# Kernel optimization log

Measured on AMD Instinct MI355X. Metric: run time of the kernel, lower is better.

The kernel has to match this reference:

```python
import jax, jax.numpy as jnp
import numpy as np

H = 32          # num_heads
D = 64          # kv_channels (head dim)
HID = 2048      # hidden_size
MAXPOS = 2048   # max_seq_length


def _rotary_table(num_pos, dim):
    # [num_pos, dim]: sin for first dim/2 cols, cos for last dim/2 cols
    inv_freq = 1.0 / (10000.0 ** (jnp.arange(0, dim, 2, dtype=jnp.float32) / dim))
    t = jnp.arange(num_pos, dtype=jnp.float32)[:, None] * inv_freq[None, :]
    return jnp.concatenate([jnp.sin(t), jnp.cos(t)], axis=1)


def _apply_rope(x, sin, cos):
    # x: [B,S,H,D]; sin,cos: [B,S,D/2]
    sin = jnp.concatenate([sin, sin], axis=-1)[:, :, None, :]  # [B,S,1,D]
    cos = jnp.concatenate([cos, cos], axis=-1)[:, :, None, :]
    half = x.shape[-1] // 2
    x1, x2 = x[..., :half], x[..., half:]
    rot = jnp.concatenate([-x2, x1], axis=-1)
    return x * cos + rot * sin


def setup_inputs() -> dict:
    key = jax.random.key(0)
    k1, k2, k3, k4 = jax.random.split(key, 4)
    B, S = 2, 2048
    hidden_states = jax.random.normal(k1, (B, S, HID), jnp.float32)
    attention_mask = jax.random.randint(k2, (B, 1, S, S), 0, 2).astype(bool)
    position_ids = jnp.broadcast_to(jnp.arange(S, dtype=jnp.int32)[None, :], (B, S))
    W_qkv = jax.random.normal(k3, (3 * H * D, HID), jnp.float32) * 0.02
    W_o = jax.random.normal(k4, (HID, H * D), jnp.float32) * 0.02
    return {"hidden_states": hidden_states, "attention_mask": attention_mask,
            "position_ids": position_ids, "W_qkv": W_qkv, "W_o": W_o}


def reference(hidden_states, attention_mask, position_ids, W_qkv, W_o):
    B, S, _ = hidden_states.shape
    # fused QKV projection (nn.Linear: x @ W.T, no bias)
    qkv = hidden_states @ W_qkv.T                       # [B,S,3*H*D]
    qkv = qkv.reshape(B, S, H, 3 * D)
    q, k, v = jnp.split(qkv, 3, axis=-1)                # each [B,S,H,D]
    sincos = _rotary_table(MAXPOS, D)[position_ids]     # [B,S,D]
    sin, cos = jnp.split(sincos, 2, axis=-1)            # [B,S,D/2] each
    q = _apply_rope(q, sin, cos)
    k = _apply_rope(k, sin, cos)
    scale = jnp.sqrt(jnp.float32(D))
    scores = jnp.einsum('bqhd,bkhd->bhqk', q, k) / scale   # [B,H,S,S]
    scores = jnp.where(attention_mask, jnp.float32(-10000.0), scores)
    weights = jax.nn.softmax(scores, axis=-1)
    attn = jnp.einsum('bhqk,bkhd->bqhd', weights, v)       # [B,S,H,D]
    attn = attn.reshape(B, S, H * D)
    return attn @ W_o.T                                    # [B,S,HID]
```

## Files before the change

kernel.cpp:

```cpp
#include <hip/hip_runtime.h>

#define B_   2
#define S_   2048
#define H_   32
#define D_   64
#define HID_ 2048

typedef unsigned short ushort_t;
typedef __attribute__((ext_vector_type(8))) short short8;
typedef __attribute__((ext_vector_type(4))) float floatx4;

typedef const __attribute__((address_space(1))) char* gas_ptr;
typedef __attribute__((address_space(3))) char* las_ptr;

__device__ __forceinline__ float bf2f(ushort_t u) {
    union { unsigned int i; float f; } v; v.i = ((unsigned int)u) << 16; return v.f;
}
__device__ __forceinline__ ushort_t f2bf(float f) {
    union { float f; unsigned int i; } v; v.f = f;
    unsigned int x = v.i;
    unsigned int r = x + 0x7fffu + ((x >> 16) & 1u);
    return (ushort_t)(r >> 16);
}

__device__ __forceinline__ float fexp2(float x) {
#if __has_builtin(__builtin_amdgcn_exp2f)
    return __builtin_amdgcn_exp2f(x);
#else
    float r; asm("v_exp_f32 %0, %1" : "=v"(r) : "v"(x)); return r;
#endif
}

__device__ __forceinline__ unsigned cvt_pk_bf16(float a, float b) {
    unsigned r;
    asm("v_cvt_pk_bf16_f32 %0, %1, %2" : "=v"(r) : "v"(a), "v"(b));
    return r;
}

__global__ __launch_bounds__(256) void cast3_f32_bf16(const float* __restrict__ in0, ushort_t* __restrict__ out0, int n0,
                                                      const float* __restrict__ in1, ushort_t* __restrict__ out1, int n1,
                                                      const float* __restrict__ in2, ushort_t* __restrict__ out2, int n2) {
    int i = blockIdx.x * 256 + threadIdx.x;
    const float* in; ushort_t* out;
    if (i < n0)            { in = in0; out = out0; }
    else if (i < n0 + n1)  { in = in1; out = out1; i -= n0; }
    else if (i < n0 + n1 + n2) { in = in2; out = out2; i -= n0 + n1; }
    else return;
    const float4* p = (const float4*)(in + (size_t)i * 8);
    float4 a = p[0], b = p[1];
    uint4 o;
    o.x = cvt_pk_bf16(a.x, a.y);
    o.y = cvt_pk_bf16(a.z, a.w);
    o.z = cvt_pk_bf16(b.x, b.y);
    o.w = cvt_pk_bf16(b.z, b.w);
    *(uint4*)(out + (size_t)i * 8) = o;
}

__global__ __launch_bounds__(256) void mask_pack(const int* __restrict__ m,
                                                 unsigned long long* __restrict__ bits) {
    int idx = blockIdx.x * 256 + threadIdx.x;
    unsigned long long bal = __ballot(m[idx] != 0);
    if ((threadIdx.x & 63) == 0) bits[idx >> 6] = bal;
}

__global__ __launch_bounds__(512, 2) void gemm256_bt(const ushort_t* __restrict__ A,
                                                     const ushort_t* __restrict__ Bm,
                                                     ushort_t* __restrict__ C,
                                                     int M, int N, int K) {
    __shared__ ushort_t lA[2][256][64];
    __shared__ ushort_t lB[2][256][64];
    const int tid  = threadIdx.x;
    const int w    = tid >> 6, lane = tid & 63;
    const int quad = lane >> 4, l16 = lane & 15;
    const int wm = w >> 2, wn = w & 3;
    const int sr = lane >> 3, ss = lane & 7;
    const int gseg = (ss ^ sr) * 8;

    const int nbx = N >> 8;
    int id  = blockIdx.x;
    int cpx = gridDim.x >> 3;
    int swz = (id & 7) * cpx + (id >> 3);
    int by = swz / nbx, bx = swz - by * nbx;
    const int m0 = by * 256, n0 = bx * 256;

    int arow[2], brow[2];
    arow[0] = w * 8;                       arow[1] = 128 + w * 8;
    brow[0] = (w >> 2) * 64 + (w & 3) * 8; brow[1] = 128 + brow[0];

    const ushort_t *gAf[2], *gAs[2], *gBf[2], *gBs[2];
#pragma unroll
    for (int c = 0; c < 2; c++) {
        gAf[c] = A  + (size_t)(m0 + arow[c] + sr) * K + gseg;
        gAs[c] = A  + (size_t)(m0 + arow[c] + 64 + sr) * K + gseg;
        gBf[c] = Bm + (size_t)(n0 + brow[c] + sr) * K + gseg;
        gBs[c] = Bm + (size_t)(n0 + brow[c] + 32 + sr) * K + gseg;
    }

#define STAGE_AF(BUF, KT) do { _Pragma("unroll") for (int c = 0; c < 2; c++) \
    __builtin_amdgcn_global_load_lds((gas_ptr)(gAf[c] + (KT)), (las_ptr)&lA[BUF][arow[c]][0], 16, 0, 0); } while (0)
#define STAGE_AS(BUF, KT) do { _Pragma("unroll") for (int c = 0; c < 2; c++) \
    __builtin_amdgcn_global_load_lds((gas_ptr)(gAs[c] + (KT)), (las_ptr)&lA[BUF][arow[c] + 64][0], 16, 0, 0); } while (0)
#define STAGE_BF(BUF, KT) do { _Pragma("unroll") for (int c = 0; c < 2; c++) \
    __builtin_amdgcn_global_load_lds((gas_ptr)(gBf[c] + (KT)), (las_ptr)&lB[BUF][brow[c]][0], 16, 0, 0); } while (0)
#define STAGE_BS(BUF, KT) do { _Pragma("unroll") for (int c = 0; c < 2; c++) \
    __builtin_amdgcn_global_load_lds((gas_ptr)(gBs[c] + (KT)), (las_ptr)&lB[BUF][brow[c] + 32][0], 16, 0, 0); } while (0)

#define LDA_(SUB, BUF) do { _Pragma("unroll") for (int mi = 0; mi < 4; mi++) \
    _Pragma("unroll") for (int ks = 0; ks < 2; ks++) \
        aF[mi][ks] = *(const short8*)&lA[BUF][wm * 128 + (SUB) * 64 + mi * 16 + l16][(((ks * 4 + quad) ^ (l16 & 7)) * 8)]; } while (0)
#define LDB_(SUB, BUF) do { _Pragma("unroll") for (int ni = 0; ni < 2; ni++) \
    _Pragma("unroll") for (int ks = 0; ks < 2; ks++) \
        bF[ni][ks] = *(const short8*)&lB[BUF][wn * 64 + (SUB) * 32 + ni * 16 + l16][(((ks * 4 + quad) ^ (l16 & 7)) * 8)]; } while (0)

#define MM_(Hh, Gg) do { _Pragma("unroll") for (int mi = 0; mi < 4; mi++) \
    _Pragma("unroll") for (int ni = 0; ni < 2; ni++) \
    _Pragma("unroll") for (int ks = 0; ks < 2; ks++) \
        acc[(Hh) * 4 + mi][(Gg) * 2 + ni] = __builtin_amdgcn_mfma_f32_16x16x32_bf16( \
            aF[mi][ks], bF[ni][ks], acc[(Hh) * 4 + mi][(Gg) * 2 + ni], 0, 0, 0); } while (0)

#define VMC6 asm volatile("s_waitcnt vmcnt(6)" ::: "memory")
#define BARR __builtin_amdgcn_s_barrier()
#define SETP1 __builtin_amdgcn_s_setprio(1)
#define SETP0 __builtin_amdgcn_s_setprio(0)

    floatx4 acc[8][4];
#pragma unroll
    for (int i = 0; i < 8; i++)
#pragma unroll
        for (int j = 0; j < 4; j++) acc[i][j] = (floatx4){0.f, 0.f, 0.f, 0.f};
    short8 aF[4][2];
    short8 bF[2][2];

    const int NT = K >> 6;
    const int NI = NT >> 1;

    STAGE_AF(0, 0); STAGE_BF(0, 0); STAGE_AS(0, 0); STAGE_BS(0, 0);
    STAGE_BF(1, 64); STAGE_AS(1, 64); STAGE_BS(1, 64);
    VMC6;
    BARR;

    for (int i = 0; i < NI; ++i) {
        const int t1k = (i << 7) + 64;
        const int t2k = t1k + 64, t3k = t1k + 128;
        const bool g2 = (t2k < K), g3 = (t3k < K);
        const bool last = (i == NI - 1);

        LDA_(0, 0); LDB_(0, 0);
        STAGE_AF(1, t1k);
        asm volatile("s_waitcnt lgkmcnt(8)" ::: "memory");
        BARR; SETP1; MM_(0, 0); SETP0;
        VMC6; BARR;
        LDA_(1, 0);
        if (g2) STAGE_BF(0, t2k);
        BARR; SETP1; MM_(1, 0); SETP0;
        VMC6; BARR;
        LDB_(1, 0);
        if (g2) STAGE_AS(0, t2k);
        BARR; SETP1; MM_(1, 1); SETP0;
        VMC6; BARR;
        LDA_(0, 0);
        if (g2) STAGE_BS(0, t2k);
        BARR; SETP1; MM_(0, 1); SETP0;
        if (last) { asm volatile("s_waitcnt vmcnt(0)" ::: "memory"); }
        else      { VMC6; }
        BARR;

        LDA_(0, 1); LDB_(0, 1);
        if (g2) STAGE_AF(0, t2k);
        asm volatile("s_waitcnt lgkmcnt(8)" ::: "memory");
        BARR; SETP1; MM_(0, 0); SETP0;
        VMC6; BARR;
        LDA_(1, 1);
        if (g3) STAGE_BF(1, t3k);
        BARR; SETP1; MM_(1, 0); SETP0;
        VMC6; BARR;
        LDB_(1, 1);
        if (g3) STAGE_AS(1, t3k);
        BARR; SETP1; MM_(1, 1); SETP0;
        VMC6; BARR;
        LDA_(0, 1);
        if (g3) STAGE_BS(1, t3k);
        BARR; SETP1; MM_(0, 1); SETP0;
        VMC6; BARR;
    }

#pragma unroll
    for (int mi = 0; mi < 8; mi++)
#pragma unroll
        for (int ni = 0; ni < 4; ni++)
#pragma unroll
            for (int r = 0; r < 4; r++) {
                int row = m0 + wm * 128 + mi * 16 + quad * 4 + r;
                int col = n0 + wn * 64 + ni * 16 + l16;
                C[(size_t)row * N + col] = f2bf(acc[mi][ni][r]);
            }
#undef STAGE_AF
#undef STAGE_AS
#undef STAGE_BF
#undef STAGE_BS
#undef LDA_
#undef LDB_
#undef MM_
#undef VMC6
#undef BARR
#undef SETP1
#undef SETP0
}

template <bool OF32>
__global__ __launch_bounds__(512, 4) void gemm_wide_bt(const ushort_t* __restrict__ A,
                                                       const ushort_t* __restrict__ Bm,
                                                       void* __restrict__ Cv,
                                                       int M, int N, int K) {
    __shared__ ushort_t lA[128][32];
    __shared__ ushort_t lB[256][32];
    const int tid  = threadIdx.x;
    const int w    = tid >> 6, lane = tid & 63;
    const int quad = lane >> 4, l16 = lane & 15;
    const int wm = w >> 2, wn = w & 3;

    const int sr = lane >> 2, ss = lane & 3;
    const int gss = ss ^ ((sr >> 1) & 3);

    const int nbx = N >> 8;
    int id  = blockIdx.x;
    int cpx = gridDim.x >> 3;
    int swz = (id & 7) * cpx + (id >> 3);
    int by = swz / nbx, bx = swz - by * nbx;
    const int m0 = by * 128, n0 = bx * 256;

    const ushort_t* gA  = A  + (size_t)(m0 + w * 16 + sr) * K + gss * 8;
    const ushort_t* gB0 = Bm + (size_t)(n0 + w * 32 + sr) * K + gss * 8;
    const ushort_t* gB1 = gB0 + (size_t)16 * K;

    const int fseg = (quad ^ ((l16 >> 1) & 3)) * 8;

    floatx4 acc[4][4];
#pragma unroll
    for (int i = 0; i < 4; i++)
#pragma unroll
        for (int j = 0; j < 4; j++) acc[i][j] = (floatx4){0.f, 0.f, 0.f, 0.f};

    for (int k0 = 0; k0 < K; k0 += 32) {
        __builtin_amdgcn_global_load_lds((gas_ptr)(gA + k0),
                                         (las_ptr)&lA[w * 16][0], 16, 0, 0);
        __builtin_amdgcn_global_load_lds((gas_ptr)(gB0 + k0),
                                         (las_ptr)&lB[w * 32][0], 16, 0, 0);
        __builtin_amdgcn_global_load_lds((gas_ptr)(gB1 + k0),
                                         (las_ptr)&lB[w * 32 + 16][0], 16, 0, 0);
        __syncthreads();

        short8 aF[4], bF[4];
#pragma unroll
        for (int mi = 0; mi < 4; mi++)
            aF[mi] = *(const short8*)&lA[wm * 64 + mi * 16 + l16][fseg];
#pragma unroll
        for (int ni = 0; ni < 4; ni++)
            bF[ni] = *(const short8*)&lB[wn * 64 + ni * 16 + l16][fseg];
#pragma unroll
        for (int mi = 0; mi < 4; mi++)
#pragma unroll
            for (int ni = 0; ni < 4; ni++)
                acc[mi][ni] = __builtin_amdgcn_mfma_f32_16x16x32_bf16(aF[mi], bF[ni], acc[mi][ni], 0, 0, 0);
        __syncthreads();
    }

#pragma unroll
    for (int mi = 0; mi < 4; mi++)
#pragma unroll
        for (int ni = 0; ni < 4; ni++)
#pragma unroll
            for (int r = 0; r < 4; r++) {
                int row = m0 + wm * 64 + mi * 16 + quad * 4 + r;
                int col = n0 + wn * 64 + ni * 16 + l16;
                if (OF32) ((float*)Cv)[(size_t)row * N + col] = acc[mi][ni][r];
                else      ((ushort_t*)Cv)[(size_t)row * N + col] = f2bf(acc[mi][ni][r]);
            }
}

__global__ __launch_bounds__(256) void rope_vt(const ushort_t* __restrict__ qkv,
                                               const int* __restrict__ pos,
                                               ushort_t* __restrict__ qr,
                                               ushort_t* __restrict__ kr,
                                               ushort_t* __restrict__ vt) {
    __shared__ ushort_t tile[64][72];
    const int bid = blockIdx.x;
    const int g  = bid >> 5;
    const int s0 = (bid & 31) * 64;
    const int b = g >> 5, h = g & 31;
    const int tid = threadIdx.x;

    {
        const int d  = tid & 63;
        const int r0 = tid >> 6;
        const int i  = d & 31;
        const int d2 = d ^ 32;
        const float inv = fexp2((float)i * -0.41524101186092985f);
        const ushort_t* qk0 = qkv + (size_t)(b * S_) * (3 * H_ * D_) + h * (3 * D_);
#pragma unroll
        for (int rr = 0; rr < 16; rr++) {
            int s = s0 + r0 + rr * 4;
            size_t qbase = (size_t)s * (3 * H_ * D_);
            float x   = bf2f(qk0[qbase + d]);
            float xp  = bf2f(qk0[qbase + d2]);
            float kx  = bf2f(qk0[qbase + 64 + d]);
            float kxp = bf2f(qk0[qbase + 64 + d2]);
            int   p   = pos[b * S_ + s];
            float t   = (float)p * inv;
            float c = cosf(t), sn = sinf(t);
            float rq = (d < 32) ? -xp : xp;
            float rk = (d < 32) ? -kxp : kxp;
            float qo = (x * c + rq * sn) * 0.18033688011112042f;
            float ko = kx * c + rk * sn;
            size_t o = ((size_t)g * S_ + s) * D_ + d;
            qr[o] = f2bf(qo);
            kr[o] = f2bf(ko);
        }
    }

    const int r = tid >> 2, c = (tid & 3) * 16;
    const ushort_t* src = qkv + ((size_t)(b * S_) + s0 + r) * (3 * H_ * D_) + h * (3 * D_) + 128 + c;
    *(short8*)&tile[r][c]     = *(const short8*)src;
    *(short8*)&tile[r][c + 8] = *(const short8*)(src + 8);
    __syncthreads();
    const int d = tid >> 2, cs = (tid & 3) * 16;
    ushort_t* dst = vt + ((size_t)g * D_ + d) * S_ + s0 + cs;
    short8 o0, o1;
#pragma unroll
    for (int j = 0; j < 8; j++) {
        o0[j] = (short)tile[cs + j][d];
        o1[j] = (short)tile[cs + 8 + j][d];
    }
    *(short8*)dst       = o0;
    *(short8*)(dst + 8) = o1;
}

__global__ __launch_bounds__(256) void attn_kernel(const ushort_t* __restrict__ qr,
                                                   const ushort_t* __restrict__ kr,
                                                   const ushort_t* __restrict__ vt,
                                                   const unsigned long long* __restrict__ mbits,
                                                   ushort_t* __restrict__ ctx) {
    __shared__ ushort_t lK[64 * 64];
    __shared__ ushort_t lV[64 * 64];
    __shared__ ushort_t lds_p[4][16][72];
    const int tid  = threadIdx.x;
    const int wave = tid >> 6, lane = tid & 63;
    const int quad = lane >> 4, l16 = lane & 15;

    const int id   = blockIdx.x;
    const int g    = (id & 7) | ((id >> 8) << 3);
    const int qblk = (id >> 3) & 31;
    const int b    = g >> 5;
    const int q0   = qblk * 64 + wave * 16;
    const size_t headBase = (size_t)g * S_ * D_;
    const unsigned long long* mrow = mbits + ((size_t)b * S_ + q0 + l16) * (S_ / 64);

    const int sr = lane >> 3, ss = lane & 7;
    const int gss = ss ^ sr;
    const ushort_t* gK0 = kr + headBase + (size_t)(wave * 16 + sr) * D_ + gss * 8;
    const ushort_t* gV0 = vt + headBase + (size_t)(wave * 16 + sr) * S_ + gss * 8;

    const int segA0 = ((quad)     ^ (l16 & 7)) * 8;
    const int segA1 = ((quad + 4) ^ (l16 & 7)) * 8;
    const int rowOff = (l16)*64;

#define STAGE_T(K0) do { _Pragma("unroll") for (int i = 0; i < 2; i++) { \
    __builtin_amdgcn_global_load_lds((gas_ptr)(gK0 + (size_t)((K0) + i * 8) * D_), \
                                     (las_ptr)(lK + (wave * 16 + i * 8) * 64), 16, 0, 0); \
    __builtin_amdgcn_global_load_lds((gas_ptr)(gV0 + (size_t)(i * 8) * S_ + (K0)), \
                                     (las_ptr)(lV + (wave * 16 + i * 8) * 64), 16, 0, 0); } } while (0)

    short8 qf0 = *(const short8*)(qr + headBase + (size_t)(q0 + l16) * D_ + quad * 8);
    short8 qf1 = *(const short8*)(qr + headBase + (size_t)(q0 + l16) * D_ + 32 + quad * 8);

    float l_st = 0.f;
    floatx4 o[4];
#pragma unroll
    for (int t = 0; t < 4; t++) o[t] = (floatx4){0.f, 0.f, 0.f, 0.f};

    STAGE_T(0);

    for (int k0 = 0; k0 < S_; k0 += 64) {
        unsigned long long mb = mrow[k0 >> 6];
        __syncthreads();

        short8 kf[4][2], vf[4][2];
#pragma unroll
        for (int t = 0; t < 4; t++) {
            kf[t][0] = *(const short8*)&lK[t * 1024 + rowOff + segA0];
            kf[t][1] = *(const short8*)&lK[t * 1024 + rowOff + segA1];
            vf[t][0] = *(const short8*)&lV[t * 1024 + rowOff + segA0];
            vf[t][1] = *(const short8*)&lV[t * 1024 + rowOff + segA1];
        }
        __syncthreads();

        if (k0 + 64 < S_) STAGE_T(k0 + 64);

        floatx4 scT[4];
#pragma unroll
        for (int t = 0; t < 4; t++) scT[t] = (floatx4){0.f, 0.f, 0.f, 0.f};
        __builtin_amdgcn_s_setprio(1);
#pragma unroll
        for (int t = 0; t < 4; t++) {
            scT[t] = __builtin_amdgcn_mfma_f32_16x16x32_bf16(kf[t][0], qf0, scT[t], 0, 0, 0);
            scT[t] = __builtin_amdgcn_mfma_f32_16x16x32_bf16(kf[t][1], qf1, scT[t], 0, 0, 0);
        }
        __builtin_amdgcn_s_setprio(0);

        unsigned mlo = (unsigned)(mb >> (quad * 4));
        unsigned mhi = (unsigned)(mb >> (quad * 4 + 32));
        float pv[4][4];
        float rs = 0.f;
#pragma unroll
        for (int t = 0; t < 4; t++) {
            unsigned msrc = (t < 2) ? mlo : mhi;
#pragma unroll
            for (int r = 0; r < 4; r++) {
                int bitpos = (t & 1) * 16 + r;
                float e = fexp2(scT[t][r]);
                e = ((msrc >> bitpos) & 1u) ? 0.f : e;
                pv[t][r] = e;
                rs += e;
            }
        }
        l_st += rs;

#pragma unroll
        for (int t = 0; t < 4; t++) {
            uint2 w;
            w.x = cvt_pk_bf16(pv[t][0], pv[t][1]);
            w.y = cvt_pk_bf16(pv[t][2], pv[t][3]);
            *(uint2*)&lds_p[wave][l16][t * 16 + quad * 4] = w;
        }
        short8 pf0 = *(const short8*)&lds_p[wave][l16][quad * 8];
        short8 pf1 = *(const short8*)&lds_p[wave][l16][32 + quad * 8];

        __builtin_amdgcn_s_setprio(1);
#pragma unroll
        for (int t = 0; t < 4; t++) {
            o[t] = __builtin_amdgcn_mfma_f32_16x16x32_bf16(pf0, vf[t][0], o[t], 0, 0, 0);
            o[t] = __builtin_amdgcn_mfma_f32_16x16x32_bf16(pf1, vf[t][1], o[t], 0, 0, 0);
        }
        __builtin_amdgcn_s_setprio(0);
    }
#undef STAGE_T

    l_st += __shfl_xor(l_st, 16);
    l_st += __shfl_xor(l_st, 32);
    float li[4];
#pragma unroll
    for (int r = 0; r < 4; r++) li[r] = 1.0f / __shfl(l_st, quad * 4 + r, 16);
#pragma unroll
    for (int t = 0; t < 4; t++)
#pragma unroll
        for (int r = 0; r < 4; r++) {
            int srow = q0 + quad * 4 + r;
            ctx[((size_t)(b * S_) + srow) * (H_ * D_) + (g & 31) * D_ + t * 16 + l16] = f2bf(o[t][r] * li[r]);
        }
}

extern "C" void kernel_launch(void* const* d_in, const int* in_sizes, int n_in,
                              void* d_out, int out_size, void* d_ws, size_t ws_size,
                              hipStream_t stream) {
    const float* hidden          = (const float*)d_in[0];
    const int* mask              = (const int*)d_in[1];
    const int* pos               = (const int*)d_in[2];
    const float* Wqkv            = (const float*)d_in[3];
    const float* Wo              = (const float*)d_in[4];
    float* out                   = (float*)d_out;

    char* ws = (char*)d_ws;
    ushort_t* qkv     = (ushort_t*)(ws);
    ushort_t* ctx     = (ushort_t*)(ws);
    unsigned long long* mbits = (unsigned long long*)(ws + 16777216);
    ushort_t* Wo_bf   = (ushort_t*)(ws + 50331648);
    ushort_t* hid_bf  = (ushort_t*)(ws + 58720256);
    ushort_t* Wqkv_bf = (ushort_t*)(ws + 75497472);
    ushort_t* q_r     = (ushort_t*)(ws + 58720256);
    ushort_t* k_r     = (ushort_t*)(ws + 75497472);
    ushort_t* v_t     = (ushort_t*)(ws + 92274688);

    {
        int n0 = (B_ * S_ * HID_) / 8;
        int n1 = (3 * H_ * D_ * HID_) / 8;
        int n2 = (HID_ * H_ * D_) / 8;
        int nb = (n0 + n1 + n2 + 255) / 256;
        cast3_f32_bf16<<<nb, 256, 0, stream>>>(hidden, hid_bf, n0,
                                               Wqkv, Wqkv_bf, n1,
                                               Wo, Wo_bf, n2);
    }

    gemm256_bt<<<((3 * H_ * D_) / 256) * ((B_ * S_) / 256), 512, 0, stream>>>(
        hid_bf, Wqkv_bf, qkv, B_ * S_, 3 * H_ * D_, HID_);

    rope_vt<<<B_ * H_ * (S_ / 64), 256, 0, stream>>>(qkv, pos, q_r, k_r, v_t);

    mask_pack<<<(B_ * S_ * S_) / 256, 256, 0, stream>>>(mask, mbits);

    attn_kernel<<<2048, 256, 0, stream>>>(q_r, k_r, v_t, mbits, ctx);

    gemm_wide_bt<true><<<(HID_ / 256) * ((B_ * S_) / 128), 512, 0, stream>>>(
        ctx, Wo_bf, out, B_ * S_, HID_, H_ * D_);
}
```

Baseline: 359.9 us.

## Process two query sub-tiles per wave to reuse staged K/V tiles

Each attention block now covers 128 query rows instead of 64, with every wave handling two 16-row query sub-tiles against each K/V tile staged in LDS. The grid is halved to 1024 blocks. This cuts K/V global-to-LDS traffic and LDS fragment reads per query row by half. In exchange it uses more registers for the doubled accumulators and score tiles, which may lower occupancy, and there are fewer blocks to spread across CUs.

```diff
diff --git a/kernel.cpp b/kernel.cpp
--- a/kernel.cpp
+++ b/kernel.cpp
@@ -348,12 +348,13 @@
     const int quad = lane >> 4, l16 = lane & 15;
 
     const int id   = blockIdx.x;
-    const int g    = (id & 7) | ((id >> 8) << 3);
-    const int qblk = (id >> 3) & 31;
+    const int g    = (id & 7) | ((id >> 7) << 3);
+    const int qblk = (id >> 3) & 15;
     const int b    = g >> 5;
-    const int q0   = qblk * 64 + wave * 16;
+    const int q0   = qblk * 128 + wave * 32;
     const size_t headBase = (size_t)g * S_ * D_;
-    const unsigned long long* mrow = mbits + ((size_t)b * S_ + q0 + l16) * (S_ / 64);
+    const unsigned long long* mrow0 = mbits + ((size_t)b * S_ + q0 + l16) * (S_ / 64);
+    const unsigned long long* mrow1 = mrow0 + (size_t)16 * (S_ / 64);
 
     const int sr = lane >> 3, ss = lane & 7;
     const int gss = ss ^ sr;
@@ -370,25 +371,52 @@
     __builtin_amdgcn_global_load_lds((gas_ptr)(gV0 + (size_t)(i * 8) * S_ + (K0)), \
                                      (las_ptr)(lV + (wave * 16 + i * 8) * 64), 16, 0, 0); } } while (0)
 
-    short8 qf0 = *(const short8*)(qr + headBase + (size_t)(q0 + l16) * D_ + quad * 8);
-    short8 qf1 = *(const short8*)(qr + headBase + (size_t)(q0 + l16) * D_ + 32 + quad * 8);
-
-    float l_st = 0.f;
-    floatx4 o[4];
-#pragma unroll
-    for (int t = 0; t < 4; t++) o[t] = (floatx4){0.f, 0.f, 0.f, 0.f};
+    short8 qf[2][2];
+#pragma unroll
+    for (int qs = 0; qs < 2; qs++) {
+        const ushort_t* qp = qr + headBase + (size_t)(q0 + qs * 16 + l16) * D_;
+        qf[qs][0] = *(const short8*)(qp + quad * 8);
+        qf[qs][1] = *(const short8*)(qp + 32 + quad * 8);
+    }
+
+    float l_st[2] = {0.f, 0.f};
+    floatx4 o[2][4];
+#pragma unroll
+    for (int qs = 0; qs < 2; qs++)
+#pragma unroll
+        for (int t = 0; t < 4; t++) o[qs][t] = (floatx4){0.f, 0.f, 0.f, 0.f};
 
     STAGE_T(0);
 
     for (int k0 = 0; k0 < S_; k0 += 64) {
-        unsigned long long mb = mrow[k0 >> 6];
+        unsigned long long mb0 = mrow0[k0 >> 6];
+        unsigned long long mb1 = mrow1[k0 >> 6];
         __syncthreads();
 
-        short8 kf[4][2], vf[4][2];
+        short8 kf[4][2];
 #pragma unroll
         for (int t = 0; t < 4; t++) {
             kf[t][0] = *(const short8*)&lK[t * 1024 + rowOff + segA0];
             kf[t][1] = *(const short8*)&lK[t * 1024 + rowOff + segA1];
+        }
+        floatx4 scT[2][4];
+#pragma unroll
+        for (int qs = 0; qs < 2; qs++)
+#pragma unroll
+            for (int t = 0; t < 4; t++) scT[qs][t] = (floatx4){0.f, 0.f, 0.f, 0.f};
+        __builtin_amdgcn_s_setprio(1);
+#pragma unroll
+        for (int qs = 0; qs < 2; qs++)
+#pragma unroll
+            for (int t = 0; t < 4; t++) {
+                scT[qs][t] = __builtin_amdgcn_mfma_f32_16x16x32_bf16(kf[t][0], qf[qs][0], scT[qs][t], 0, 0, 0);
+                scT[qs][t] = __builtin_amdgcn_mfma_f32_16x16x32_bf16(kf[t][1], qf[qs][1], scT[qs][t], 0, 0, 0);
+            }
+        __builtin_amdgcn_s_setprio(0);
+
+        short8 vf[4][2];
+#pragma unroll
+        for (int t = 0; t < 4; t++) {
             vf[t][0] = *(const short8*)&lV[t * 1024 + rowOff + segA0];
             vf[t][1] = *(const short8*)&lV[t * 1024 + rowOff + segA1];
         }
@@ -396,67 +424,64 @@
 
         if (k0 + 64 < S_) STAGE_T(k0 + 64);
 
-        floatx4 scT[4];
-#pragma unroll
-        for (int t = 0; t < 4; t++) scT[t] = (floatx4){0.f, 0.f, 0.f, 0.f};
-        __builtin_amdgcn_s_setprio(1);
-#pragma unroll
-        for (int t = 0; t < 4; t++) {
-            scT[t] = __builtin_amdgcn_mfma_f32_16x16x32_bf16(kf[t][0], qf0, scT[t], 0, 0, 0);
-            scT[t] = __builtin_amdgcn_mfma_f32_16x16x32_bf16(kf[t][1], qf1, scT[t], 0, 0, 0);
+#pragma unroll
+        for (int qs = 0; qs < 2; qs++) {
+            unsigned long long mb = qs ? mb1 : mb0;
+            unsigned mlo = (unsigned)(mb >> (quad * 4));
+            unsigned mhi = (unsigned)(mb >> (quad * 4 + 32));
+            float pv[4][4];
+            float rs = 0.f;
+#pragma unroll
+            for (int t = 0; t < 4; t++) {
+                unsigned msrc = (t < 2) ? mlo : mhi;
+#pragma unroll
+                for (int r = 0; r < 4; r++) {
+                    int bitpos = (t & 1) * 16 + r;
+                    float e = fexp2(scT[qs][t][r]);
+                    e = ((msrc >> bitpos) & 1u) ? 0.f : e;
+                    pv[t][r] = e;
+                    rs += e;
+                }
+            }
+            l_st[qs] += rs;
+
+#pragma unroll
+            for (int t = 0; t < 4; t++) {
+                uint2 w;
+                w.x = cvt_pk_bf16(pv[t][0], pv[t][1]);
+                w.y = cvt_pk_bf16(pv[t][2], pv[t][3]);
+                *(uint2*)&lds_p[wave][l16][t * 16 + quad * 4] = w;
+            }
+            short8 pf0 = *(const short8*)&lds_p[wave][l16][quad * 8];
+            short8 pf1 = *(const short8*)&lds_p[wave][l16][32 + quad * 8];
+
+            __builtin_amdgcn_s_setprio(1);
+#pragma unroll
+            for (int t = 0; t < 4; t++) {
+                o[qs][t] = __builtin_amdgcn_mfma_f32_16x16x32_bf16(pf0, vf[t][0], o[qs][t], 0, 0, 0);
+                o[qs][t] = __builtin_amdgcn_mfma_f32_16x16x32_bf16(pf1, vf[t][1], o[qs][t], 0, 0, 0);
+            }
+            __builtin_amdgcn_s_setprio(0);
         }
-        __builtin_amdgcn_s_setprio(0);
-
-        unsigned mlo = (unsigned)(mb >> (quad * 4));
-        unsigned mhi = (unsigned)(mb >> (quad * 4 + 32));
-        float pv[4][4];
-        float rs = 0.f;
-#pragma unroll
-        for (int t = 0; t < 4; t++) {
-            unsigned msrc = (t < 2) ? mlo : mhi;
+    }
+#undef STAGE_T
+
+#pragma unroll
+    for (int qs = 0; qs < 2; qs++) {
+        float ls = l_st[qs];
+        ls += __shfl_xor(ls, 16);
+        ls += __shfl_xor(ls, 32);
+        float li[4];
+#pragma unroll
+        for (int r = 0; r < 4; r++) li[r] = 1.0f / __shfl(ls, quad * 4 + r, 16);
+#pragma unroll
+        for (int t = 0; t < 4; t++)
 #pragma unroll
             for (int r = 0; r < 4; r++) {
-                int bitpos = (t & 1) * 16 + r;
-                float e = fexp2(scT[t][r]);
-                e = ((msrc >> bitpos) & 1u) ? 0.f : e;
-                pv[t][r] = e;
-                rs += e;
-            }
-        }
-        l_st += rs;
-
-#pragma unroll
-        for (int t = 0; t < 4; t++) {
-            uint2 w;
-            w.x = cvt_pk_bf16(pv[t][0], pv[t][1]);
-            w.y = cvt_pk_bf16(pv[t][2], pv[t][3]);
-            *(uint2*)&lds_p[wave][l16][t * 16 + quad * 4] = w;
-        }
-        short8 pf0 = *(const short8*)&lds_p[wave][l16][quad * 8];
-        short8 pf1 = *(const short8*)&lds_p[wave][l16][32 + quad * 8];
-
-        __builtin_amdgcn_s_setprio(1);
-#pragma unroll
-        for (int t = 0; t < 4; t++) {
-            o[t] = __builtin_amdgcn_mfma_f32_16x16x32_bf16(pf0, vf[t][0], o[t], 0, 0, 0);
-            o[t] = __builtin_amdgcn_mfma_f32_16x16x32_bf16(pf1, vf[t][1], o[t], 0, 0, 0);
-        }
-        __builtin_amdgcn_s_setprio(0);
-    }
-#undef STAGE_T
-
-    l_st += __shfl_xor(l_st, 16);
-    l_st += __shfl_xor(l_st, 32);
-    float li[4];
-#pragma unroll
-    for (int r = 0; r < 4; r++) li[r] = 1.0f / __shfl(l_st, quad * 4 + r, 16);
-#pragma unroll
-    for (int t = 0; t < 4; t++)
-#pragma unroll
-        for (int r = 0; r < 4; r++) {
-            int srow = q0 + quad * 4 + r;
-            ctx[((size_t)(b * S_) + srow) * (H_ * D_) + (g & 31) * D_ + t * 16 + l16] = f2bf(o[t][r] * li[r]);
-        }
+                int srow = q0 + qs * 16 + quad * 4 + r;
+                ctx[((size_t)(b * S_) + srow) * (H_ * D_) + (g & 31) * D_ + t * 16 + l16] = f2bf(o[qs][t][r] * li[r]);
+            }
+    }
 }
 
 extern "C" void kernel_launch(void* const* d_in, const int* in_sizes, int n_in,
@@ -497,7 +522,7 @@
 
     mask_pack<<<(B_ * S_ * S_) / 256, 256, 0, stream>>>(mask, mbits);
 
-    attn_kernel<<<2048, 256, 0, stream>>>(q_r, k_r, v_t, mbits, ctx);
+    attn_kernel<<<1024, 256, 0, stream>>>(q_r, k_r, v_t, mbits, ctx);
 
     gemm_wide_bt<true><<<(HID_ / 256) * ((B_ * S_) / 128), 512, 0, stream>>>(
         ctx, Wo_bf, out, B_ * S_, HID_, H_ * D_);
```

Measured after the change: 365.4 us. About the same (+1.5%).
